# Kernel optimization log

Measured on AMD Instinct MI355X. Metric: run time of the kernel, lower is better.

## Reference

```python
import jax, jax.numpy as jnp
import numpy as np

TEMPERATURE = 0.2
NUMBER_CLASSES = 1000
LOSS_SCALE = 0.001

N, F = 8192, 256
M = 20000
DEPTH = 4


def setup_inputs() -> dict:
    key = jax.random.key(0)
    k1, k2, k3, k4 = jax.random.split(key, 4)
    gt_labels = jax.random.randint(k1, (N,), 0, NUMBER_CLASSES, dtype=jnp.int32)
    box_features = jax.random.normal(k2, (N, F), dtype=jnp.float32)
    memory = jax.random.normal(k3, (M, F), dtype=jnp.float32)
    trace_idx = jax.random.randint(k4, (NUMBER_CLASSES, DEPTH), 0, M, dtype=jnp.int32)
    return {"gt_labels": gt_labels, "box_features": box_features,
            "memory": memory, "trace_idx": trace_idx}


def reference(gt_labels, box_features, memory, trace_idx):
    # logits[i, j] = dot(f_i, m_j) / T  (the nested python loops fused into one GEMM)
    logits = jnp.einsum('nf,mf->nm', box_features, memory) / TEMPERATURE  # [N, M]
    # fenmu = sum_j exp(logits)  ->  log(fenmu) = logsumexp
    lse = jax.nn.logsumexp(logits, axis=-1)  # [N]
    # gather the trace entries for each item's label: [N, DEPTH]
    traces = trace_idx[gt_labels]  # [N, DEPTH]
    sel = jnp.take_along_axis(logits, traces, axis=1)  # [N, DEPTH]
    depth_w = jnp.arange(DEPTH, dtype=logits.dtype)  # gj = depth
    sum_gj = depth_w.sum()  # sum of layer weights (0+1+2+3)
    # per item: -sum_d gj * log(sim_d / fenmu) / sum_gj
    per_item = -jnp.sum((sel - lse[:, None]) * depth_w, axis=-1) / sum_gj  # [N]
    # background filter: items with label == number_classes contribute nothing
    fg = (gt_labels != NUMBER_CLASSES)
    loss = jnp.sum(jnp.where(fg, per_item, 0.0)) * LOSS_SCALE
    return loss
```

## Files before the change

kernel.cpp:

```cpp
#include <hip/hip_runtime.h>
#include <hip/hip_bf16.h>
#include <stdint.h>

#define NROWS 8192
#define FDIM 256
#define MCOLS 20000
#define NT32 625
#define MSPLIT 16
#define NCLS 1000
#define LOG2E 1.44269504088896f
#define LN2   0.69314718055994f


typedef short short8 __attribute__((ext_vector_type(8)));
typedef float f32x4 __attribute__((ext_vector_type(4)));

typedef __attribute__((address_space(3))) unsigned int lds_u32;
typedef const __attribute__((address_space(1))) unsigned int glb_u32;

__device__ __forceinline__ float ex2(float x) {
    float r;
    asm("v_exp_f32 %0, %1" : "=v"(r) : "v"(x));
    return r;
}

__device__ __forceinline__ unsigned short f2bf(float x) {
    unsigned u = __float_as_uint(x);
    unsigned r = (u + 0x7FFFu + ((u >> 16) & 1u)) >> 16;
    return (unsigned short)r;
}

__global__ void conv_kernel(const float* __restrict__ in, unsigned short* __restrict__ out,
                            int n4, float scale) {
    int idx = blockIdx.x * blockDim.x + threadIdx.x;
    if (idx >= n4) return;
    float4 v = ((const float4*)in)[idx];
    ushort4 o;
    o.x = f2bf(v.x * scale); o.y = f2bf(v.y * scale);
    o.z = f2bf(v.z * scale); o.w = f2bf(v.w * scale);
    ((ushort4*)out)[idx] = o;
}

__global__ void sel_kernel(const int* __restrict__ gt, const float* __restrict__ F,
                           const float* __restrict__ Mem, const int* __restrict__ trace,
                           float* __restrict__ wsel) {
    int lane = threadIdx.x & 63, wid = threadIdx.x >> 6;
    int i = blockIdx.x * 4 + wid;
    int label = gt[i];
    float w = 0.0f;
    if (label >= 0 && label < NCLS) {
        float4 fv = ((const float4*)(F + (size_t)i * FDIM))[lane];
        #pragma unroll
        for (int d = 1; d <= 3; ++d) {
            int tr = trace[label * 4 + d];
            float4 mv = ((const float4*)(Mem + (size_t)tr * FDIM))[lane];
            float dot = fv.x*mv.x + fv.y*mv.y + fv.z*mv.z + fv.w*mv.w;
            #pragma unroll
            for (int off = 32; off >= 1; off >>= 1) dot += __shfl_xor(dot, off, 64);
            w += (float)d * dot;
        }
    }
    if (lane == 0) wsel[i] = w * 5.0f;
}

__global__ __launch_bounds__(256, 2) void lse_gemm(
        const unsigned short* __restrict__ Fb, const unsigned short* __restrict__ Mb,
        float* __restrict__ pm, float* __restrict__ ps) {
    __shared__ __align__(16) char smem[2 * 16384];

    const int split  = blockIdx.x;
    const int rowblk = blockIdx.y;
    const int tid  = threadIdx.x;
    const int lane = tid & 63, wid = tid >> 6;
    const int r0 = lane & 15, hi = lane >> 4;
    const int rowbase = rowblk * 128 + wid * 32;

    short8 a[2][8];
    #pragma unroll
    for (int rf = 0; rf < 2; ++rf)
        #pragma unroll
        for (int kk = 0; kk < 8; ++kk)
            a[rf][kk] = *(const short8*)(Fb + (size_t)(rowbase + rf*16 + r0) * FDIM + kk*32 + hi*8);

    float m[8], s[8];
    #pragma unroll
    for (int q = 0; q < 8; ++q) { m[q] = -3.0e38f; s[q] = 0.0f; }

    const int t0 = (split * NT32) / MSPLIT;
    const int t1 = ((split + 1) * NT32) / MSPLIT;

    int srcoff[4];
    #pragma unroll
    for (int c = 0; c < 4; ++c) {
        const int g = (wid * 4 + c) * 64 + lane;
        const int j = g >> 5, o = g & 31;
        srcoff[c] = j * 512 + ((o ^ (j & 7)) << 4);
    }

#define STAGE(buf, t)                                                              \
    do {                                                                           \
        const char* srcT = (const char*)Mb + (size_t)(t) * 16384;                  \
        _Pragma("unroll")                                                          \
        for (int c = 0; c < 4; ++c) {                                              \
            __builtin_amdgcn_global_load_lds(                                      \
                (glb_u32*)(srcT + srcoff[c]),                                      \
                (lds_u32*)((char*)smem + (buf) * 16384 + (wid * 4 + c) * 1024),    \
                16, 0, 0);                                                         \
        }                                                                          \
    } while (0)

    const int swzr = (r0 & 7) << 4;
    int roff[8];
    #pragma unroll
    for (int kk = 0; kk < 8; ++kk)
        roff[kk] = r0 * 512 + ((kk * 64 + hi * 16) ^ swzr);

#define BODY(BUF, t, pref)                                                         \
    do {                                                                           \
        if (pref) STAGE((BUF) ^ 1, (t) + 1);                                       \
        f32x4 acc00 = {0,0,0,0}, acc01 = {0,0,0,0}, acc10 = {0,0,0,0}, acc11 = {0,0,0,0}; \
        _Pragma("unroll")                                                          \
        for (int kk = 0; kk < 8; ++kk) {                                           \
            short8 b0 = *(const short8*)(smem + roff[kk] + (BUF) * 16384);         \
            short8 b1 = *(const short8*)(smem + roff[kk] + (BUF) * 16384 + 8192);  \
            acc00 = __builtin_amdgcn_mfma_f32_16x16x32_bf16(a[0][kk], b0, acc00, 0, 0, 0); \
            acc10 = __builtin_amdgcn_mfma_f32_16x16x32_bf16(a[1][kk], b0, acc10, 0, 0, 0); \
            acc01 = __builtin_amdgcn_mfma_f32_16x16x32_bf16(a[0][kk], b1, acc01, 0, 0, 0); \
            acc11 = __builtin_amdgcn_mfma_f32_16x16x32_bf16(a[1][kk], b1, acc11, 0, 0, 0); \
        }                                                                          \
        _Pragma("unroll")                                                          \
        for (int r = 0; r < 4; ++r) {                                              \
            { float v0 = acc00[r], v1 = acc01[r];                                  \
              float nm = fmaxf(fmaxf(m[r], v0), v1);                               \
              float em = ex2(m[r] - nm), e0 = ex2(v0 - nm), e1 = ex2(v1 - nm);     \
              s[r] = fmaf(s[r], em, e0 + e1); m[r] = nm; }                         \
            { float v0 = acc10[r], v1 = acc11[r];                                  \
              float nm = fmaxf(fmaxf(m[4 + r], v0), v1);                           \
              float em = ex2(m[4 + r] - nm), e0 = ex2(v0 - nm), e1 = ex2(v1 - nm); \
              s[4 + r] = fmaf(s[4 + r], em, e0 + e1); m[4 + r] = nm; }             \
        }                                                                          \
        __syncthreads();                                                           \
    } while (0)

    STAGE(0, t0);
    __syncthreads();

    int t = t0;
    while (t + 2 <= t1) {
        BODY(0, t, true);
        BODY(1, t + 1, (t + 2 < t1));
        t += 2;
    }
    if (t < t1) BODY(0, t, false);

#undef BODY
#undef STAGE

    #pragma unroll
    for (int off = 1; off <= 8; off <<= 1) {
        #pragma unroll
        for (int q = 0; q < 8; ++q) {
            float om = __shfl_xor(m[q], off, 64);
            float os = __shfl_xor(s[q], off, 64);
            float nm = fmaxf(m[q], om);
            float sn = fmaf(s[q], ex2(m[q] - nm), os * ex2(om - nm));
            m[q] = nm; s[q] = sn;
        }
    }
    if (r0 == 0) {
        #pragma unroll
        for (int rf = 0; rf < 2; ++rf)
            #pragma unroll
            for (int r = 0; r < 4; ++r) {
                int row = rowbase + rf * 16 + hi * 4 + r;
                pm[split * NROWS + row] = m[rf * 4 + r];
                ps[split * NROWS + row] = s[rf * 4 + r];
            }
    }
}

__global__ void finalize_kernel(const int* __restrict__ gt, const float* __restrict__ wsel,
                                const float* __restrict__ pm, const float* __restrict__ ps,
                                float* __restrict__ bpart) {
    int tid = threadIdx.x;
    int i = blockIdx.x * 256 + tid;
    float mv[MSPLIT];
    float M = -3.0e38f;
    #pragma unroll
    for (int k = 0; k < MSPLIT; ++k) { mv[k] = pm[k * NROWS + i]; M = fmaxf(M, mv[k]); }
    float S = 0.0f;
    #pragma unroll
    for (int k = 0; k < MSPLIT; ++k) S += ps[k * NROWS + i] * ex2(mv[k] - M);
    float lse = (M + __log2f(S)) * LN2;
    int label = gt[i];
    float per = (label >= 0 && label < NCLS) ? (lse - wsel[i] * (1.0f / 6.0f)) : 0.0f;
    #pragma unroll
    for (int off = 32; off >= 1; off >>= 1) per += __shfl_xor(per, off, 64);
    __shared__ float red[4];
    int lane = tid & 63, wid = tid >> 6;
    if (lane == 0) red[wid] = per;
    __syncthreads();
    if (tid == 0) bpart[blockIdx.x] = red[0] + red[1] + red[2] + red[3];
}

__global__ void sum_kernel(const float* __restrict__ bpart, float* __restrict__ out) {
    int tid = threadIdx.x;
    float v = (tid < 32) ? bpart[tid] : 0.0f;
    #pragma unroll
    for (int off = 32; off >= 1; off >>= 1) v += __shfl_xor(v, off, 64);
    if (tid == 0) out[0] = 0.001f * v;
}

extern "C" void kernel_launch(void* const* d_in, const int* in_sizes, int n_in,
                              void* d_out, int out_size, void* d_ws, size_t ws_size,
                              hipStream_t stream) {
    const int*   gt    = (const int*)d_in[0];
    const float* F     = (const float*)d_in[1];
    const float* Mem   = (const float*)d_in[2];
    const int*   trace = (const int*)d_in[3];
    float* out = (float*)d_out;

    char* w = (char*)d_ws;
    unsigned short* Mb = (unsigned short*)w;
    unsigned short* Fb = (unsigned short*)(w + 10240000);
    float* wsel  = (float*)(w + 14434304);
    float* pm    = (float*)(w + 14467072);
    float* ps    = (float*)(w + 14991360);
    float* bpart = (float*)(w + 15515648);

    conv_kernel<<<dim3((MCOLS * FDIM / 4) / 256), dim3(256), 0, stream>>>(Mem, Mb, MCOLS * FDIM / 4, 1.0f);
    conv_kernel<<<dim3((NROWS * FDIM / 4) / 256), dim3(256), 0, stream>>>(F, Fb, NROWS * FDIM / 4, 5.0f * LOG2E);
    sel_kernel<<<dim3(NROWS / 4), dim3(256), 0, stream>>>(gt, F, Mem, trace, wsel);
    lse_gemm<<<dim3(MSPLIT, NROWS / 128), dim3(256), 0, stream>>>(Fb, Mb, pm, ps);
    finalize_kernel<<<dim3(NROWS / 256), dim3(256), 0, stream>>>(gt, wsel, pm, ps, bpart);
    sum_kernel<<<dim3(1), dim3(64), 0, stream>>>(bpart, out);
}
```

Measured before the change: 113.0 us.

## Switch LSE GEMM to 32x32x16 MFMA with memory-row-major accumulator layout

Replaces four 16x16x32 MFMAs per k-step with one 32x32x16 MFMA per k-step, swapping operands so each lane's 16 accumulator values belong to a single feature row. The online max/sum-exp then runs once per lane per tile with a 16-wide reduction, and the end-of-kernel shuffle reduction shrinks to a single xor-32 step. The LDS swizzle is widened to a full XOR over 32 chunks, s_setprio is raised around the MFMA loop, and the prefetch is issued before each compute block. The aim is lower per-tile softmax and reduction overhead and better MFMA issue efficiency. The cost is larger register use from the 16-element A fragment array and the 16-wide accumulator.

```diff
diff --git a/kernel.cpp b/kernel.cpp
--- a/kernel.cpp
+++ b/kernel.cpp
@@ -13,7 +13,7 @@
 
 
 typedef short short8 __attribute__((ext_vector_type(8)));
-typedef float f32x4 __attribute__((ext_vector_type(4)));
+typedef float f32x16 __attribute__((ext_vector_type(16)));
 
 typedef __attribute__((address_space(3))) unsigned int lds_u32;
 typedef const __attribute__((address_space(1))) unsigned int glb_u32;
@@ -72,19 +72,16 @@
     const int rowblk = blockIdx.y;
     const int tid  = threadIdx.x;
     const int lane = tid & 63, wid = tid >> 6;
-    const int r0 = lane & 15, hi = lane >> 4;
+    const int r0 = lane & 31;
+    const int hi = lane >> 5;
     const int rowbase = rowblk * 128 + wid * 32;
 
-    short8 a[2][8];
-    #pragma unroll
-    for (int rf = 0; rf < 2; ++rf)
-        #pragma unroll
-        for (int kk = 0; kk < 8; ++kk)
-            a[rf][kk] = *(const short8*)(Fb + (size_t)(rowbase + rf*16 + r0) * FDIM + kk*32 + hi*8);
-
-    float m[8], s[8];
-    #pragma unroll
-    for (int q = 0; q < 8; ++q) { m[q] = -3.0e38f; s[q] = 0.0f; }
+    short8 a[16];
+    #pragma unroll
+    for (int kk = 0; kk < 16; ++kk)
+        a[kk] = *(const short8*)(Fb + (size_t)(rowbase + r0) * FDIM + kk * 16 + hi * 8);
+
+    float m = -3.0e38f, s = 0.0f;
 
     const int t0 = (split * NT32) / MSPLIT;
     const int t1 = ((split + 1) * NT32) / MSPLIT;
@@ -94,52 +91,52 @@
     for (int c = 0; c < 4; ++c) {
         const int g = (wid * 4 + c) * 64 + lane;
         const int j = g >> 5, o = g & 31;
-        srcoff[c] = j * 512 + ((o ^ (j & 7)) << 4);
-    }
-
-#define STAGE(buf, t)                                                              \
+        srcoff[c] = j * 512 + ((o ^ j) << 4);
+    }
+
+#define STAGE(BUF, t)                                                              \
     do {                                                                           \
         const char* srcT = (const char*)Mb + (size_t)(t) * 16384;                  \
         _Pragma("unroll")                                                          \
         for (int c = 0; c < 4; ++c) {                                              \
             __builtin_amdgcn_global_load_lds(                                      \
                 (glb_u32*)(srcT + srcoff[c]),                                      \
-                (lds_u32*)((char*)smem + (buf) * 16384 + (wid * 4 + c) * 1024),    \
+                (lds_u32*)(smem + (BUF) * 16384 + (wid * 4 + c) * 1024),           \
                 16, 0, 0);                                                         \
         }                                                                          \
     } while (0)
 
-    const int swzr = (r0 & 7) << 4;
-    int roff[8];
-    #pragma unroll
-    for (int kk = 0; kk < 8; ++kk)
-        roff[kk] = r0 * 512 + ((kk * 64 + hi * 16) ^ swzr);
-
-#define BODY(BUF, t, pref)                                                         \
+    int roff[16];
+    #pragma unroll
+    for (int kk = 0; kk < 16; ++kk)
+        roff[kk] = r0 * 512 + ((((kk << 1) | hi) ^ r0) << 4);
+
+#define BODYC(BUF)                                                                 \
     do {                                                                           \
-        if (pref) STAGE((BUF) ^ 1, (t) + 1);                                       \
-        f32x4 acc00 = {0,0,0,0}, acc01 = {0,0,0,0}, acc10 = {0,0,0,0}, acc11 = {0,0,0,0}; \
+        f32x16 acc = {0,0,0,0,0,0,0,0,0,0,0,0,0,0,0,0};                            \
+        __builtin_amdgcn_s_setprio(1);                                             \
         _Pragma("unroll")                                                          \
-        for (int kk = 0; kk < 8; ++kk) {                                           \
-            short8 b0 = *(const short8*)(smem + roff[kk] + (BUF) * 16384);         \
-            short8 b1 = *(const short8*)(smem + roff[kk] + (BUF) * 16384 + 8192);  \
-            acc00 = __builtin_amdgcn_mfma_f32_16x16x32_bf16(a[0][kk], b0, acc00, 0, 0, 0); \
-            acc10 = __builtin_amdgcn_mfma_f32_16x16x32_bf16(a[1][kk], b0, acc10, 0, 0, 0); \
-            acc01 = __builtin_amdgcn_mfma_f32_16x16x32_bf16(a[0][kk], b1, acc01, 0, 0, 0); \
-            acc11 = __builtin_amdgcn_mfma_f32_16x16x32_bf16(a[1][kk], b1, acc11, 0, 0, 0); \
+        for (int kk = 0; kk < 16; ++kk) {                                          \
+            short8 b = *(const short8*)(smem + (BUF) * 16384 + roff[kk]);          \
+            acc = __builtin_amdgcn_mfma_f32_32x32x16_bf16(b, a[kk], acc, 0, 0, 0); \
         }                                                                          \
+        __builtin_amdgcn_s_setprio(0);                                             \
+        float x0 = fmaxf(fmaxf(acc[0],  acc[1]),  acc[2]);                         \
+        float x1 = fmaxf(fmaxf(acc[3],  acc[4]),  acc[5]);                         \
+        float x2 = fmaxf(fmaxf(acc[6],  acc[7]),  acc[8]);                         \
+        float x3 = fmaxf(fmaxf(acc[9],  acc[10]), acc[11]);                        \
+        float x4 = fmaxf(fmaxf(acc[12], acc[13]), acc[14]);                        \
+        float x5 = fmaxf(fmaxf(x0, x1), x2);                                       \
+        float x6 = fmaxf(fmaxf(x3, x4), acc[15]);                                  \
+        float nm = fmaxf(fmaxf(x5, x6), m);                                        \
+        float p0 = 0.f, p1 = 0.f, p2 = 0.f, p3 = 0.f;                              \
         _Pragma("unroll")                                                          \
-        for (int r = 0; r < 4; ++r) {                                              \
-            { float v0 = acc00[r], v1 = acc01[r];                                  \
-              float nm = fmaxf(fmaxf(m[r], v0), v1);                               \
-              float em = ex2(m[r] - nm), e0 = ex2(v0 - nm), e1 = ex2(v1 - nm);     \
-              s[r] = fmaf(s[r], em, e0 + e1); m[r] = nm; }                         \
-            { float v0 = acc10[r], v1 = acc11[r];                                  \
-              float nm = fmaxf(fmaxf(m[4 + r], v0), v1);                           \
-              float em = ex2(m[4 + r] - nm), e0 = ex2(v0 - nm), e1 = ex2(v1 - nm); \
-              s[4 + r] = fmaf(s[4 + r], em, e0 + e1); m[4 + r] = nm; }             \
+        for (int i = 0; i < 16; i += 4) {                                          \
+            p0 += ex2(acc[i]     - nm); p1 += ex2(acc[i + 1] - nm);                \
+            p2 += ex2(acc[i + 2] - nm); p3 += ex2(acc[i + 3] - nm);                \
         }                                                                          \
-        __syncthreads();                                                           \
+        s = fmaf(s, ex2(m - nm), (p0 + p1) + (p2 + p3));                           \
+        m = nm;                                                                    \
     } while (0)
 
     STAGE(0, t0);
@@ -147,35 +144,28 @@
 
     int t = t0;
     while (t + 2 <= t1) {
-        BODY(0, t, true);
-        BODY(1, t + 1, (t + 2 < t1));
+        STAGE(1, t + 1);
+        BODYC(0);
+        __syncthreads();
+        if (t + 2 < t1) STAGE(0, t + 2);
+        BODYC(1);
+        __syncthreads();
         t += 2;
     }
-    if (t < t1) BODY(0, t, false);
-
-#undef BODY
+    if (t < t1) BODYC(0);
+
+#undef BODYC
 #undef STAGE
 
-    #pragma unroll
-    for (int off = 1; off <= 8; off <<= 1) {
-        #pragma unroll
-        for (int q = 0; q < 8; ++q) {
-            float om = __shfl_xor(m[q], off, 64);
-            float os = __shfl_xor(s[q], off, 64);
-            float nm = fmaxf(m[q], om);
-            float sn = fmaf(s[q], ex2(m[q] - nm), os * ex2(om - nm));
-            m[q] = nm; s[q] = sn;
+    {
+        float om = __shfl_xor(m, 32, 64);
+        float os = __shfl_xor(s, 32, 64);
+        float nm = fmaxf(m, om);
+        float sf = fmaf(s, ex2(m - nm), os * ex2(om - nm));
+        if (lane < 32) {
+            pm[split * NROWS + rowbase + lane] = nm;
+            ps[split * NROWS + rowbase + lane] = sf;
         }
-    }
-    if (r0 == 0) {
-        #pragma unroll
-        for (int rf = 0; rf < 2; ++rf)
-            #pragma unroll
-            for (int r = 0; r < 4; ++r) {
-                int row = rowbase + rf * 16 + hi * 4 + r;
-                pm[split * NROWS + row] = m[rf * 4 + r];
-                ps[split * NROWS + row] = s[rf * 4 + r];
-            }
     }
 }
 
```

Measured after the change: 109.2 us. 3.4% less time.
